# Kernel tuning notes

Hardware: AMD Instinct MI355X
Metric: run time of the kernel (lower is better)

Reference implementation:

```python
import jax, jax.numpy as jnp
import numpy as np

HIDDEN = 4096
N_HEADS = 32
N_KV = 8
HEAD_DIM = HIDDEN // N_HEADS  # 128
EPS = 1e-6
THETA = 10000.0
T = 2048


def _rms_norm(x, w, eps=EPS):
    # x: [T, H, D]; normalize over last dim
    var = jnp.mean(jnp.square(x), axis=-1, keepdims=True)
    return x * jax.lax.rsqrt(var + eps) * w


def _rope(pos, q, k, theta=THETA):
    # pos: [T] int; q: [T, Hq, D]; k: [T, Hk, D]  (rotate-half / NeoX style)
    d = q.shape[-1]
    inv_freq = 1.0 / (theta ** (jnp.arange(0, d, 2, dtype=jnp.float32) / d))  # [D/2]
    ang = pos.astype(jnp.float32)[:, None] * inv_freq  # [T, D/2]
    cos = jnp.cos(ang)[:, None, :]  # [T, 1, D/2]
    sin = jnp.sin(ang)[:, None, :]

    def rot(x):
        x1, x2 = jnp.split(x, 2, axis=-1)
        return jnp.concatenate([x1 * cos - x2 * sin, x2 * cos + x1 * sin], axis=-1)

    return rot(q), rot(k)


def setup_inputs() -> dict:
    key = jax.random.key(0)
    ks = jax.random.split(key, 4)
    x = jax.random.normal(ks[0], (T, HIDDEN), dtype=jnp.float32)
    pos = jnp.arange(T, dtype=jnp.int32)
    qkv_w = jax.random.normal(ks[1], (HIDDEN, HEAD_DIM * (N_HEADS + 2 * N_KV)), dtype=jnp.float32) * (HIDDEN ** -0.5)
    q_norm_w = jnp.ones((HEAD_DIM,), dtype=jnp.float32)
    k_norm_w = jnp.ones((HEAD_DIM,), dtype=jnp.float32)
    o_w = jax.random.normal(ks[2], (HIDDEN, HIDDEN), dtype=jnp.float32) * (HIDDEN ** -0.5)
    return {"x": x, "pos": pos, "qkv_w": qkv_w, "q_norm_w": q_norm_w,
            "k_norm_w": k_norm_w, "o_w": o_w}


def reference(x, pos, qkv_w, q_norm_w, k_norm_w, o_w):
    q_size = N_HEADS * HEAD_DIM
    kv_size = N_KV * HEAD_DIM
    qkv = x @ qkv_w  # [T, q+2kv]
    q, k, v = jnp.split(qkv, [q_size, q_size + kv_size], axis=-1)
    q = q.reshape(T, N_HEADS, HEAD_DIM)
    k = k.reshape(T, N_KV, HEAD_DIM)
    v = v.reshape(T, N_KV, HEAD_DIM)
    # per-head RMSNorm on q/k (qkv_bias=False path)
    q = _rms_norm(q, q_norm_w)
    k = _rms_norm(k, k_norm_w)
    q, k = _rope(pos, q, k)
    # GQA: expand kv heads to query heads
    g = N_HEADS // N_KV
    k = jnp.repeat(k, g, axis=1)  # [T, Hq, D]
    v = jnp.repeat(v, g, axis=1)
    scale = HEAD_DIM ** -0.5
    scores = jnp.einsum('thd,shd->hts', q, k) * scale  # [H, T, T]
    causal = jnp.tril(jnp.ones((T, T), dtype=bool))
    scores = jnp.where(causal[None], scores, jnp.finfo(scores.dtype).min)
    p = jax.nn.softmax(scores, axis=-1)
    o = jnp.einsum('hts,shd->thd', p, v).reshape(T, HIDDEN)
    return o @ o_w
```

## Files before the change

### kernel.cpp

```cpp
#include <hip/hip_runtime.h>
#include <hip/hip_bf16.h>

using u16 = unsigned short;
typedef __bf16 bf16x8 __attribute__((ext_vector_type(8)));
typedef float f32x4 __attribute__((ext_vector_type(4)));
typedef u16 u16x8 __attribute__((ext_vector_type(8)));
typedef u16 u16x4 __attribute__((ext_vector_type(4)));

constexpr int T_SEQ = 2048;
constexpr int HID   = 4096;
constexpr int NH    = 32;
constexpr int NKV   = 8;
constexpr int HD    = 128;
constexpr int QKVN  = 6144;

__device__ __forceinline__ u16 f2b(float x) {
  return __builtin_bit_cast(u16, __float2bfloat16(x));
}
__device__ __forceinline__ float b2f(u16 u) {
  return __builtin_bit_cast(float, (unsigned int)u << 16);
}
__device__ __forceinline__ bf16x8 load8(const u16* p) {
  return __builtin_bit_cast(bf16x8, *reinterpret_cast<const u16x8*>(p));
}
__device__ __forceinline__ f32x4 mfma16(bf16x8 a, bf16x8 b, f32x4 c) {
  return __builtin_amdgcn_mfma_f32_16x16x32_bf16(a, b, c, 0, 0, 0);
}
__device__ __forceinline__ void gload_lds16(const u16* src, u16* dst) {
  __builtin_amdgcn_global_load_lds((const __attribute__((address_space(1))) void*)src,
                                   (__attribute__((address_space(3))) void*)dst, 16, 0, 0);
}
#define BAR() asm volatile("s_barrier" ::: "memory")

__global__ __launch_bounds__(256) void k_cast_bf16(const float* __restrict__ in,
                                                   u16* __restrict__ out, int n4) {
  int i = blockIdx.x * 256 + threadIdx.x;
  if (i < n4) {
    float4 v = reinterpret_cast<const float4*>(in)[i];
    u16x4 o;
    o.x = f2b(v.x); o.y = f2b(v.y); o.z = f2b(v.z); o.w = f2b(v.w);
    reinterpret_cast<u16x4*>(out)[i] = o;
  }
}

__global__ __launch_bounds__(256) void k_transpose_cast(const float* __restrict__ in,
                                                        u16* __restrict__ out,
                                                        int R, int C) {
  __shared__ float tile[32][33];
  int cc = blockIdx.x << 5, rr = blockIdx.y << 5;
  int lx = threadIdx.x & 31, ly = threadIdx.x >> 5;
#pragma unroll
  for (int i = 0; i < 32; i += 8)
    tile[ly + i][lx] = in[(size_t)(rr + ly + i) * C + cc + lx];
  __syncthreads();
#pragma unroll
  for (int i = 0; i < 32; i += 8)
    out[(size_t)(cc + ly + i) * R + rr + lx] = f2b(tile[lx][ly + i]);
}

template <int N, int K, typename OutT>
__global__ __launch_bounds__(512, 2) void k_gemm8(const u16* __restrict__ A,
                                                  const u16* __restrict__ B,
                                                  OutT* __restrict__ C) {
  __shared__ u16 sA[2][256 * 64];
  __shared__ u16 sB[2][256 * 64];
  const int tid = threadIdx.x;
  const int wid = tid >> 6, lane = tid & 63;
  const int g = lane >> 4, c = lane & 15;
  const int wm = wid >> 2, wn = wid & 3;

  const int NWG = (T_SEQ / 256) * (N / 256);
  const int wg = (blockIdx.x & 7) * (NWG / 8) + (blockIdx.x >> 3);
  const int NBc = N / 256;
  const int row0 = (wg / NBc) * 256, col0 = (wg % NBc) * 256;
  const int NT = K / 64;

  auto stage_half = [&](int h) {
    const int T = h >> 2, k = h & 3;
    const int buf = T & 1;
    const int kk = T * 64;
    const u16* gbase = (k < 2) ? A : B;
    const int grow0 = ((k < 2) ? row0 : col0) + (k & 1) * 128;
    u16* lbase = ((k < 2) ? sA[buf] : sB[buf]) + (k & 1) * (128 * 64);
#pragma unroll
    for (int i = 0; i < 2; ++i) {
      int L = i * 512 + tid;
      int r = L >> 3, seg = L & 7;
      const u16* src = gbase + (size_t)(grow0 + r) * K + kk + ((seg ^ (r & 7)) * 8);
      u16* dst = lbase + (i * 512 + wid * 64) * 8;
      gload_lds16(src, dst);
    }
  };

  f32x4 acc[8][4] = {};
  bf16x8 a[4][2], b[4][2];

  auto read_a = [&](int buf, int mbase) {
#pragma unroll
    for (int m = 0; m < 4; ++m) {
      int r = wm * 128 + (mbase + m) * 16 + c;
#pragma unroll
      for (int k2 = 0; k2 < 2; ++k2) {
        int q = k2 * 4 + g;
        a[m][k2] = load8(sA[buf] + r * 64 + ((q ^ (r & 7)) * 8));
      }
    }
  };
  auto read_b = [&](int buf, int nbase) {
#pragma unroll
    for (int n = 0; n < 2; ++n) {
      int r = wn * 64 + (nbase + n) * 16 + c;
#pragma unroll
      for (int k2 = 0; k2 < 2; ++k2) {
        int q = k2 * 4 + g;
        b[nbase + n][k2] = load8(sB[buf] + r * 64 + ((q ^ (r & 7)) * 8));
      }
    }
  };
  auto quad = [&](int mb, int nb) {
    __builtin_amdgcn_s_setprio(1);
#pragma unroll
    for (int m = 0; m < 4; ++m)
#pragma unroll
      for (int n = 0; n < 2; ++n)
#pragma unroll
        for (int k2 = 0; k2 < 2; ++k2)
          acc[mb + m][nb + n] = mfma16(a[m][k2], b[nb + n][k2], acc[mb + m][nb + n]);
    __builtin_amdgcn_s_setprio(0);
  };

  stage_half(0); stage_half(1); stage_half(2); stage_half(3); stage_half(4);
  asm volatile("s_waitcnt vmcnt(2)" ::: "memory");
  BAR();

  for (int kt = 0; kt < NT; ++kt) {
    const int buf = kt & 1;
    read_a(buf, 0); read_b(buf, 0);
    if (4 * kt + 5 < 4 * NT) stage_half(4 * kt + 5);
    BAR();
    quad(0, 0);
    BAR();
    read_b(buf, 2);
    if (4 * kt + 6 < 4 * NT) stage_half(4 * kt + 6);
    BAR();
    quad(0, 2);
    BAR();
    read_a(buf, 4);
    if (4 * kt + 7 < 4 * NT) stage_half(4 * kt + 7);
    BAR();
    quad(4, 0);
    BAR();
    if (4 * kt + 8 < 4 * NT) stage_half(4 * kt + 8);
    asm volatile("s_waitcnt vmcnt(2)" ::: "memory");
    BAR();
    quad(4, 2);
    BAR();
  }

#pragma unroll
  for (int m = 0; m < 8; ++m) {
    int grow0 = row0 + wm * 128 + m * 16 + g * 4;
#pragma unroll
    for (int n = 0; n < 4; ++n) {
      int gcol = col0 + wn * 64 + n * 16 + c;
#pragma unroll
      for (int j = 0; j < 4; ++j) {
        float v = acc[m][n][j];
        if constexpr (sizeof(OutT) == 2)
          C[(size_t)(grow0 + j) * N + gcol] = f2b(v);
        else
          C[(size_t)(grow0 + j) * N + gcol] = v;
      }
    }
  }
}

__global__ __launch_bounds__(256) void k_normrope(const u16* __restrict__ qkv,
                                                  const int* __restrict__ pos,
                                                  const float* __restrict__ qw,
                                                  const float* __restrict__ kw,
                                                  u16* __restrict__ qo,
                                                  u16* __restrict__ ko,
                                                  u16* __restrict__ vo) {
  int t = blockIdx.x;
  int wid = threadIdx.x >> 6, lane = threadIdx.x & 63;
  int h = blockIdx.y * 4 + wid;
  const u16* src = qkv + (size_t)t * QKVN + h * HD;
  float x1 = b2f(src[lane]), x2 = b2f(src[lane + 64]);
  float ss = x1 * x1 + x2 * x2;
#pragma unroll
  for (int m = 1; m < 64; m <<= 1) ss += __shfl_xor(ss, m);
  float sc = rsqrtf(ss * (1.0f / HD) + 1e-6f);
  if (h < 40) {
    const float* w = (h < NH) ? qw : kw;
    float y1 = x1 * sc * w[lane], y2 = x2 * sc * w[lane + 64];
    float p = (float)pos[t];
    float inv = exp2f((float)lane * (-13.287712379549449f / 64.0f));
    float ang = p * inv;
    float sn, cs;
    sincosf(ang, &sn, &cs);
    float o1 = y1 * cs - y2 * sn;
    float o2 = y2 * cs + y1 * sn;
    if (h < NH) {
      o1 *= 0.08838834764831845f;
      o2 *= 0.08838834764831845f;
      u16* dst = qo + ((size_t)t * NH + h) * HD;
      dst[lane] = f2b(o1);
      dst[lane + 64] = f2b(o2);
    } else {
      u16* dst = ko + ((size_t)t * NKV + (h - NH)) * HD;
      dst[lane] = f2b(o1);
      dst[lane + 64] = f2b(o2);
    }
  } else {
    u16* dst = vo + ((size_t)t * NKV + (h - 40)) * HD;
    dst[lane] = f2b(x1);
    dst[lane + 64] = f2b(x2);
  }
}

__global__ __launch_bounds__(256) void k_transpose_v(const u16* __restrict__ vb,
                                                     u16* __restrict__ vt) {
  __shared__ u16 tile[32][33];
  int tt = blockIdx.x << 5, dd = blockIdx.y << 5, h = blockIdx.z;
  int lx = threadIdx.x & 31, ly = threadIdx.x >> 5;
#pragma unroll
  for (int i = 0; i < 32; i += 8)
    tile[ly + i][lx] = vb[((size_t)(tt + ly + i) * NKV + h) * HD + dd + lx];
  __syncthreads();
#pragma unroll
  for (int i = 0; i < 32; i += 8)
    vt[((size_t)h * HD + dd + ly + i) * T_SEQ + tt + lx] = tile[lx][ly + i];
}

__global__ __launch_bounds__(256) void k_attn(const u16* __restrict__ qb,
                                              const u16* __restrict__ kbg,
                                              const u16* __restrict__ vtg,
                                              u16* __restrict__ out) {
  __shared__ u16 sK[2][64 * 128];
  __shared__ u16 sV[2][128 * 64];
  const int wid = threadIdx.x >> 6, lane = threadIdx.x & 63;
  const int h = blockIdx.y, hk = h >> 2;
  const int qt = gridDim.x - 1 - blockIdx.x;
  const int ntiles = qt + 1;
  const int qb0 = qt * 64 + wid * 16;
  const int g = lane >> 4, c = lane & 15;

  auto stage = [&](int buf, int kvb) {
#pragma unroll
    for (int ii = 0; ii < 4; ++ii) {
      int i = wid * 4 + ii;
      {
        int r = i * 4 + (lane >> 4);
        int slot = lane & 15;
        const u16* src = kbg + ((size_t)(kvb + r) * NKV + hk) * HD + ((slot ^ (r & 15)) * 8);
        gload_lds16(src, (u16*)((char*)sK[buf] + i * 1024));
      }
      {
        int d = i * 8 + (lane >> 3);
        int slot3 = lane & 7;
        const u16* src = vtg + ((size_t)hk * HD + d) * T_SEQ + kvb + ((slot3 ^ (d & 7)) * 8);
        gload_lds16(src, (u16*)((char*)sV[buf] + i * 1024));
      }
    }
  };

  bf16x8 qf[4];
  const u16* qrow = qb + ((size_t)(qb0 + c) * NH + h) * HD;
#pragma unroll
  for (int kc = 0; kc < 4; ++kc) qf[kc] = load8(qrow + kc * 32 + g * 8);

  f32x4 accO[8] = {};
  float m_ = -1e30f, l_ = 0.f;
  const int tq = qb0 + c;

  const int gh = g >> 1, gl4 = 4 * (g & 1), cx = c & 7;
  const int e0 = ((0 + gh) ^ cx) * 8 + gl4;
  const int e1 = ((2 + gh) ^ cx) * 8 + gl4;
  const int e2 = ((4 + gh) ^ cx) * 8 + gl4;
  const int e3 = ((6 + gh) ^ cx) * 8 + gl4;

  stage(0, 0);
  __syncthreads();

  for (int kt = 0; kt < ntiles; ++kt) {
    const int kvb = kt * 64;
    const int cur = kt & 1;
    if (kt + 1 < ntiles) stage(cur ^ 1, kvb + 64);

    f32x4 s[4];
#pragma unroll
    for (int tt = 0; tt < 4; ++tt) {
      const u16* kr = sK[cur] + (tt * 16 + c) * 128;
      f32x4 st = {0.f, 0.f, 0.f, 0.f};
#pragma unroll
      for (int kc = 0; kc < 4; ++kc) {
        int slot = (kc * 4 + g) ^ c;
        st = mfma16(load8(kr + slot * 8), qf[kc], st);
      }
      s[tt] = st;
    }

    float vmax = -1e30f;
#pragma unroll
    for (int tt = 0; tt < 4; ++tt)
#pragma unroll
      for (int j = 0; j < 4; ++j) {
        int tk = kvb + tt * 16 + 4 * g + j;
        float v = (tk <= tq) ? s[tt][j] : -1e30f;
        s[tt][j] = v;
        vmax = fmaxf(vmax, v);
      }
    vmax = fmaxf(vmax, __shfl_xor(vmax, 16));
    vmax = fmaxf(vmax, __shfl_xor(vmax, 32));
    float mn = fmaxf(m_, vmax);
    float a = __expf(m_ - mn);
    float ps = 0.f;
#pragma unroll
    for (int tt = 0; tt < 4; ++tt)
#pragma unroll
      for (int j = 0; j < 4; ++j) {
        float p = __expf(s[tt][j] - mn);
        s[tt][j] = p;
        ps += p;
      }
    ps += __shfl_xor(ps, 16);
    ps += __shfl_xor(ps, 32);
    l_ = l_ * a + ps;
    m_ = mn;

    float aq[4];
#pragma unroll
    for (int j = 0; j < 4; ++j) aq[j] = __shfl(a, 20 * g + j);
#pragma unroll
    for (int c2 = 0; c2 < 8; ++c2)
#pragma unroll
      for (int j = 0; j < 4; ++j) accO[c2][j] *= aq[j];

    u16x8 p0u, p1u;
#pragma unroll
    for (int j = 0; j < 4; ++j) {
      p0u[j]     = f2b(s[0][j]);
      p0u[j + 4] = f2b(s[1][j]);
      p1u[j]     = f2b(s[2][j]);
      p1u[j + 4] = f2b(s[3][j]);
    }
    bf16x8 p0 = __builtin_bit_cast(bf16x8, p0u);
    bf16x8 p1 = __builtin_bit_cast(bf16x8, p1u);

#pragma unroll
    for (int c2 = 0; c2 < 8; ++c2) {
      const u16* vr = sV[cur] + (c2 * 16 + c) * 64;
      u16x4 va  = *reinterpret_cast<const u16x4*>(vr + e0);
      u16x4 vb4 = *reinterpret_cast<const u16x4*>(vr + e1);
      u16x4 vc4 = *reinterpret_cast<const u16x4*>(vr + e2);
      u16x4 vd  = *reinterpret_cast<const u16x4*>(vr + e3);
      u16x8 v0u, v1u;
#pragma unroll
      for (int j = 0; j < 4; ++j) {
        v0u[j] = va[j];  v0u[j + 4] = vb4[j];
        v1u[j] = vc4[j]; v1u[j + 4] = vd[j];
      }
      accO[c2] = mfma16(p0, __builtin_bit_cast(bf16x8, v0u), accO[c2]);
      accO[c2] = mfma16(p1, __builtin_bit_cast(bf16x8, v1u), accO[c2]);
    }

    __syncthreads();
  }

  float lq[4];
#pragma unroll
  for (int j = 0; j < 4; ++j) lq[j] = 1.0f / __shfl(l_, 20 * g + j);
#pragma unroll
  for (int c2 = 0; c2 < 8; ++c2)
#pragma unroll
    for (int j = 0; j < 4; ++j) {
      float o = accO[c2][j] * lq[j];
      out[(size_t)(qb0 + 4 * g + j) * HID + h * HD + c2 * 16 + c] = f2b(o);
    }
}

extern "C" void kernel_launch(void* const* d_in, const int* in_sizes, int n_in,
                              void* d_out, int out_size, void* d_ws, size_t ws_size,
                              hipStream_t stream) {
  (void)in_sizes; (void)n_in; (void)out_size; (void)ws_size;
  const float* x      = (const float*)d_in[0];
  const int*   pos    = (const int*)d_in[1];
  const float* qkv_w  = (const float*)d_in[2];
  const float* qnw    = (const float*)d_in[3];
  const float* knw    = (const float*)d_in[4];
  const float* ow     = (const float*)d_in[5];
  float* out = (float*)d_out;
  char* ws = (char*)d_ws;

  u16* xb   = (u16*)(ws + 0);
  u16* attn = (u16*)(ws + 0);
  char* B0 = ws + 16777216;
  u16* qkv_wt = (u16*)B0;
  u16* qbuf = (u16*)(B0 + 0);
  u16* kbuf = (u16*)(B0 + 16777216);
  u16* vbuf = (u16*)(B0 + 20971520);
  u16* vtb  = (u16*)(B0 + 25165824);
  char* C0 = ws + 67108864;
  u16* qkvb = (u16*)C0;
  u16* o_wt = (u16*)C0;

  k_cast_bf16<<<dim3((T_SEQ * HID / 4 + 255) / 256), 256, 0, stream>>>(x, xb, T_SEQ * HID / 4);
  k_transpose_cast<<<dim3(QKVN / 32, HID / 32), 256, 0, stream>>>(qkv_w, qkv_wt, HID, QKVN);
  k_gemm8<QKVN, HID, u16><<<dim3((T_SEQ / 256) * (QKVN / 256)), 512, 0, stream>>>(xb, qkv_wt, qkvb);
  k_normrope<<<dim3(T_SEQ, 12), 256, 0, stream>>>(qkvb, pos, qnw, knw, qbuf, kbuf, vbuf);
  k_transpose_v<<<dim3(T_SEQ / 32, HD / 32, NKV), 256, 0, stream>>>(vbuf, vtb);
  k_transpose_cast<<<dim3(HID / 32, HID / 32), 256, 0, stream>>>(ow, o_wt, HID, HID);
  k_attn<<<dim3(T_SEQ / 64, NH), 256, 0, stream>>>(qbuf, kbuf, vtb, attn);
  k_gemm8<HID, HID, float><<<dim3((T_SEQ / 256) * (HID / 256)), 512, 0, stream>>>(attn, o_wt, out);
}
```

Before: 650.5 us.

## Shrink GEMM tile to 256x128 with reworked staging pipeline

Changes the bf16 GEMM macro-tile from 256x256 to 256x128. Warps move from a 2x4 to a 4x2 layout, each owning a 64x64 sub-tile, and global-to-LDS staging is rewritten into 64-row chunks prefetched across the four phases. The aim is to double the workgroup count (the 4096-wide GEMM goes from 128 to 256 blocks) so the many CUs are better filled, and to cut LDS and register use. The cost is less operand reuse per block and more total global traffic.

```diff
diff --git a/kernel.cpp b/kernel.cpp
--- a/kernel.cpp
+++ b/kernel.cpp
@@ -63,103 +63,90 @@
                                                   const u16* __restrict__ B,
                                                   OutT* __restrict__ C) {
   __shared__ u16 sA[2][256 * 64];
-  __shared__ u16 sB[2][256 * 64];
+  __shared__ u16 sB[2][128 * 64];
   const int tid = threadIdx.x;
   const int wid = tid >> 6, lane = tid & 63;
   const int g = lane >> 4, c = lane & 15;
-  const int wm = wid >> 2, wn = wid & 3;
-
-  const int NWG = (T_SEQ / 256) * (N / 256);
+  const int wm = wid >> 1, wn = wid & 1;
+
+  const int NWG = (T_SEQ / 256) * (N / 128);
   const int wg = (blockIdx.x & 7) * (NWG / 8) + (blockIdx.x >> 3);
-  const int NBc = N / 256;
-  const int row0 = (wg / NBc) * 256, col0 = (wg % NBc) * 256;
+  const int NBc = N / 128;
+  const int row0 = (wg / NBc) * 256, col0 = (wg % NBc) * 128;
   const int NT = K / 64;
 
-  auto stage_half = [&](int h) {
-    const int T = h >> 2, k = h & 3;
-    const int buf = T & 1;
-    const int kk = T * 64;
-    const u16* gbase = (k < 2) ? A : B;
-    const int grow0 = ((k < 2) ? row0 : col0) + (k & 1) * 128;
-    u16* lbase = ((k < 2) ? sA[buf] : sB[buf]) + (k & 1) * (128 * 64);
-#pragma unroll
-    for (int i = 0; i < 2; ++i) {
-      int L = i * 512 + tid;
-      int r = L >> 3, seg = L & 7;
-      const u16* src = gbase + (size_t)(grow0 + r) * K + kk + ((seg ^ (r & 7)) * 8);
-      u16* dst = lbase + (i * 512 + wid * 64) * 8;
-      gload_lds16(src, dst);
-    }
+  const int rl = lane >> 3, seg = lane & 7;
+
+  auto stage_chunk = [&](int T, int ch) {
+    if (T >= NT) return;
+    const int buf = T & 1, kk = T * 64;
+    const bool isA = ch < 4;
+    const int rbase = isA ? ch * 64 : (ch - 4) * 64;
+    const int row = rbase + wid * 8 + rl;
+    const int grow = (isA ? row0 : col0) + row;
+    const u16* src = (isA ? A : B) + (size_t)grow * K + kk + ((seg ^ rl) * 8);
+    u16* dst = (isA ? sA[buf] : sB[buf]) + rbase * 64 + wid * 512;
+    gload_lds16(src, dst);
   };
 
-  f32x4 acc[8][4] = {};
+  f32x4 acc[4][4] = {};
   bf16x8 a[4][2], b[4][2];
 
-  auto read_a = [&](int buf, int mbase) {
-#pragma unroll
-    for (int m = 0; m < 4; ++m) {
-      int r = wm * 128 + (mbase + m) * 16 + c;
-#pragma unroll
-      for (int k2 = 0; k2 < 2; ++k2) {
-        int q = k2 * 4 + g;
-        a[m][k2] = load8(sA[buf] + r * 64 + ((q ^ (r & 7)) * 8));
-      }
+  auto read_a2 = [&](int buf, int m0) {
+#pragma unroll
+    for (int m = m0; m < m0 + 2; ++m) {
+      int r = wm * 64 + m * 16 + c;
+#pragma unroll
+      for (int k2 = 0; k2 < 2; ++k2)
+        a[m][k2] = load8(sA[buf] + r * 64 + (((k2 * 4 + g) ^ (c & 7)) * 8));
     }
   };
-  auto read_b = [&](int buf, int nbase) {
-#pragma unroll
-    for (int n = 0; n < 2; ++n) {
-      int r = wn * 64 + (nbase + n) * 16 + c;
-#pragma unroll
-      for (int k2 = 0; k2 < 2; ++k2) {
-        int q = k2 * 4 + g;
-        b[nbase + n][k2] = load8(sB[buf] + r * 64 + ((q ^ (r & 7)) * 8));
-      }
+  auto read_b2 = [&](int buf, int n0) {
+#pragma unroll
+    for (int n = n0; n < n0 + 2; ++n) {
+      int r = wn * 64 + n * 16 + c;
+#pragma unroll
+      for (int k2 = 0; k2 < 2; ++k2)
+        b[n][k2] = load8(sB[buf] + r * 64 + (((k2 * 4 + g) ^ (c & 7)) * 8));
     }
   };
-  auto quad = [&](int mb, int nb) {
+  auto quad = [&](int mh, int nh) {
     __builtin_amdgcn_s_setprio(1);
 #pragma unroll
-    for (int m = 0; m < 4; ++m)
-#pragma unroll
-      for (int n = 0; n < 2; ++n)
+    for (int m = 2 * mh; m < 2 * mh + 2; ++m)
+#pragma unroll
+      for (int n = 2 * nh; n < 2 * nh + 2; ++n)
 #pragma unroll
         for (int k2 = 0; k2 < 2; ++k2)
-          acc[mb + m][nb + n] = mfma16(a[m][k2], b[nb + n][k2], acc[mb + m][nb + n]);
+          acc[m][n] = mfma16(a[m][k2], b[n][k2], acc[m][n]);
     __builtin_amdgcn_s_setprio(0);
   };
 
-  stage_half(0); stage_half(1); stage_half(2); stage_half(3); stage_half(4);
+#pragma unroll
+  for (int ch = 0; ch < 6; ++ch) stage_chunk(0, ch);
+  stage_chunk(1, 0); stage_chunk(1, 1);
   asm volatile("s_waitcnt vmcnt(2)" ::: "memory");
   BAR();
 
   for (int kt = 0; kt < NT; ++kt) {
     const int buf = kt & 1;
-    read_a(buf, 0); read_b(buf, 0);
-    if (4 * kt + 5 < 4 * NT) stage_half(4 * kt + 5);
-    BAR();
-    quad(0, 0);
-    BAR();
-    read_b(buf, 2);
-    if (4 * kt + 6 < 4 * NT) stage_half(4 * kt + 6);
-    BAR();
-    quad(0, 2);
-    BAR();
-    read_a(buf, 4);
-    if (4 * kt + 7 < 4 * NT) stage_half(4 * kt + 7);
-    BAR();
-    quad(4, 0);
-    BAR();
-    if (4 * kt + 8 < 4 * NT) stage_half(4 * kt + 8);
-    asm volatile("s_waitcnt vmcnt(2)" ::: "memory");
-    BAR();
-    quad(4, 2);
-    BAR();
+    read_a2(buf, 0); read_b2(buf, 0);
+    stage_chunk(kt + 1, 2); stage_chunk(kt + 1, 3);
+    BAR(); quad(0, 0); BAR();
+    read_b2(buf, 2);
+    stage_chunk(kt + 1, 4); stage_chunk(kt + 1, 5);
+    BAR(); quad(0, 1); BAR();
+    read_a2(buf, 2);
+    BAR(); quad(1, 0); BAR();
+    stage_chunk(kt + 2, 0); stage_chunk(kt + 2, 1);
+    if (kt + 2 < NT) { asm volatile("s_waitcnt vmcnt(2)" ::: "memory"); }
+    else             { asm volatile("s_waitcnt vmcnt(0)" ::: "memory"); }
+    BAR(); quad(1, 1); BAR();
   }
 
 #pragma unroll
-  for (int m = 0; m < 8; ++m) {
-    int grow0 = row0 + wm * 128 + m * 16 + g * 4;
+  for (int m = 0; m < 4; ++m) {
+    int grow0 = row0 + wm * 64 + m * 16 + g * 4;
 #pragma unroll
     for (int n = 0; n < 4; ++n) {
       int gcol = col0 + wn * 64 + n * 16 + c;
@@ -407,10 +394,10 @@
 
   k_cast_bf16<<<dim3((T_SEQ * HID / 4 + 255) / 256), 256, 0, stream>>>(x, xb, T_SEQ * HID / 4);
   k_transpose_cast<<<dim3(QKVN / 32, HID / 32), 256, 0, stream>>>(qkv_w, qkv_wt, HID, QKVN);
-  k_gemm8<QKVN, HID, u16><<<dim3((T_SEQ / 256) * (QKVN / 256)), 512, 0, stream>>>(xb, qkv_wt, qkvb);
+  k_gemm8<QKVN, HID, u16><<<dim3((T_SEQ / 256) * (QKVN / 128)), 512, 0, stream>>>(xb, qkv_wt, qkvb);
   k_normrope<<<dim3(T_SEQ, 12), 256, 0, stream>>>(qkvb, pos, qnw, knw, qbuf, kbuf, vbuf);
   k_transpose_v<<<dim3(T_SEQ / 32, HD / 32, NKV), 256, 0, stream>>>(vbuf, vtb);
   k_transpose_cast<<<dim3(HID / 32, HID / 32), 256, 0, stream>>>(ow, o_wt, HID, HID);
   k_attn<<<dim3(T_SEQ / 64, NH), 256, 0, stream>>>(qbuf, kbuf, vtb, attn);
-  k_gemm8<HID, HID, float><<<dim3((T_SEQ / 256) * (HID / 256)), 512, 0, stream>>>(attn, o_wt, out);
-}
+  k_gemm8<HID, HID, float><<<dim3((T_SEQ / 256) * (HID / 128)), 512, 0, stream>>>(attn, o_wt, out);
+}
```

Measured after the change: 675.0 us. +3.8%, slower.
